# Optimization experiments

Measured on AMD Instinct MI355X. Metric: run time of the kernel, lower is better.

Reference implementation:

```python
import jax, jax.numpy as jnp
import numpy as np

REL_CONTEXT = 0.2  # default forward arg

def setup_inputs() -> dict:
    key = jax.random.key(0)
    ks = jax.random.split(key, 8)
    B, M, D = 4096, 2, 2048
    return {
        "x": jax.random.normal(ks[0], (B, M, D), jnp.float32),
        "sub_type_ids": jax.random.randint(ks[1], (B, M), 0, M),
        "modal_weights": jnp.ones((M,), jnp.float32),
        "emb_table": jax.random.normal(ks[2], (M, D), jnp.float32),
        "Wt": jax.random.normal(ks[3], (D, D), jnp.float32) * (1.0 / np.sqrt(D)),
        "bt": jax.random.normal(ks[4], (D,), jnp.float32) * 0.01,
        "Wrc": jax.random.normal(ks[5], (1, D), jnp.float32) * (1.0 / np.sqrt(D)),
        "brc": jax.random.normal(ks[6], (1,), jnp.float32) * 0.01,
    }

def reference(x, sub_type_ids, modal_weights, emb_table, Wt, bt, Wrc, brc):
    B = x.shape[0]
    D = emb_table.shape[1]
    x = x.reshape(B, -1, D)  # [B, M, D]
    # relational gate: Linear(D->1) on a constant vector filled with 0.2 -> scalar
    rc = jnp.full((D,), REL_CONTEXT, dtype=x.dtype)
    zeta = jax.nn.sigmoid(rc @ Wrc.T + brc)  # [1]
    sub = emb_table[sub_type_ids]  # [B, M, D] embedding lookup
    # fused: per-modality Linear + ReLU (replaces the B*M python loop)
    t = jax.nn.relu(jnp.einsum('bmd,ed->bme', x + sub, Wt) + bt)  # [B, M, D]
    h = modal_weights[None, :, None] * t * zeta[0]
    # dropout is identity in eval mode; final ReLU as in the original
    return jax.nn.relu(h)
```

## Files before the change

kernel.cpp:

```cpp
#include <hip/hip_runtime.h>
#include <hip/hip_bf16.h>
#include <math.h>

#define MROWS 8192
#define KDIM  2048
#define NDIM  2048

#define BM 256
#define BN 128
#define BK 64

typedef short  v8s __attribute__((ext_vector_type(8)));
typedef float  v4f __attribute__((ext_vector_type(4)));

#define A_OFF   0ull
#define W_OFF   ((unsigned long long)MROWS * KDIM * 2ull)
#define MWZ_OFF (W_OFF + (unsigned long long)NDIM * KDIM * 2ull)

__device__ inline unsigned short f2bf(float f) {
    __hip_bfloat16 h = __float2bfloat16(f);
    return *reinterpret_cast<unsigned short*>(&h);
}

__global__ __launch_bounds__(256) void prep_kernel(
    const float* __restrict__ x, const int* __restrict__ ids,
    const float* __restrict__ mw, const float* __restrict__ emb,
    const float* __restrict__ Wrc, const float* __restrict__ brc,
    const float* __restrict__ Wt,
    unsigned short* __restrict__ Abf, unsigned short* __restrict__ Wbf,
    float* __restrict__ mwz)
{
    const int tid = threadIdx.x;

    if (blockIdx.x == 0) {
        __shared__ float red[256];
        float s = 0.f;
        for (int d = tid; d < KDIM; d += 256) s += Wrc[d];
        red[tid] = s;
        __syncthreads();
        for (int off = 128; off > 0; off >>= 1) {
            if (tid < off) red[tid] += red[tid + off];
            __syncthreads();
        }
        if (tid == 0) {
            float zeta = 1.0f / (1.0f + expf(-(0.2f * red[0] + brc[0])));
            mwz[0] = mw[0] * zeta;
            mwz[1] = mw[1] * zeta;
        }
    }

    const int groupsA = MROWS * KDIM / 8;
    for (int g = blockIdx.x * 256 + tid; g < groupsA; g += gridDim.x * 256) {
        const int row = g >> 8;
        const int off = (g & 255) << 3;
        const int st  = ids[row];
        const float4* xp = (const float4*)(x   + (size_t)row * KDIM + off);
        const float4* ep = (const float4*)(emb + (size_t)st  * KDIM + off);
        float4 x0 = xp[0], x1 = xp[1];
        float4 e0 = ep[0], e1 = ep[1];
        v8s o;
        o[0] = (short)f2bf(x0.x + e0.x);
        o[1] = (short)f2bf(x0.y + e0.y);
        o[2] = (short)f2bf(x0.z + e0.z);
        o[3] = (short)f2bf(x0.w + e0.w);
        o[4] = (short)f2bf(x1.x + e1.x);
        o[5] = (short)f2bf(x1.y + e1.y);
        o[6] = (short)f2bf(x1.z + e1.z);
        o[7] = (short)f2bf(x1.w + e1.w);
        *(v8s*)(Abf + (size_t)g * 8) = o;
    }

    const int groupsW = NDIM * KDIM / 8;
    for (int g = blockIdx.x * 256 + tid; g < groupsW; g += gridDim.x * 256) {
        const float4* wp = (const float4*)(Wt + (size_t)g * 8);
        float4 w0 = wp[0], w1 = wp[1];
        v8s o;
        o[0] = (short)f2bf(w0.x); o[1] = (short)f2bf(w0.y);
        o[2] = (short)f2bf(w0.z); o[3] = (short)f2bf(w0.w);
        o[4] = (short)f2bf(w1.x); o[5] = (short)f2bf(w1.y);
        o[6] = (short)f2bf(w1.z); o[7] = (short)f2bf(w1.w);
        *(v8s*)(Wbf + (size_t)g * 8) = o;
    }
}

__global__ __launch_bounds__(256, 2) void gemm_kernel(
    const unsigned short* __restrict__ Abf,
    const unsigned short* __restrict__ Wbf,
    const float* __restrict__ bt,
    const float* __restrict__ mwz,
    float* __restrict__ out)
{
    __shared__ __align__(16) unsigned short lA[BM * BK];
    __shared__ __align__(16) unsigned short lB[BN * BK];

    const int tid  = threadIdx.x;
    const int lane = tid & 63;
    const int wave = tid >> 6;
    const int wr   = wave & 1;
    const int wc   = wave >> 1;
    const int quad = lane >> 4;
    const int mcol = lane & 15;

    const int br = blockIdx.x;
    const int bc = blockIdx.y;

    v4f acc[8][4];
    const v4f vzero = {0.f, 0.f, 0.f, 0.f};
    #pragma unroll
    for (int i = 0; i < 8; i++)
        #pragma unroll
        for (int j = 0; j < 4; j++) acc[i][j] = vzero;

    const unsigned short* gA = Abf + (size_t)(br * BM) * KDIM;
    const unsigned short* gB = Wbf + (size_t)(bc * BN) * KDIM;

    for (int kt = 0; kt < KDIM; kt += BK) {
        #pragma unroll
        for (int q = 0; q < 8; q++) {
            const int f   = q * 256 + tid;
            const int row = f >> 3;
            const int ch  = (f & 7) ^ (row & 7);
            const unsigned short* ga = gA + (size_t)row * KDIM + kt + ch * 8;
            __builtin_amdgcn_global_load_lds(
                (const __attribute__((address_space(1))) void*)ga,
                (__attribute__((address_space(3))) void*)(&lA[(size_t)f * 8]),
                16, 0, 0);
        }
        #pragma unroll
        for (int q = 0; q < 4; q++) {
            const int f   = q * 256 + tid;
            const int row = f >> 3;
            const int ch  = (f & 7) ^ (row & 7);
            const unsigned short* gb = gB + (size_t)row * KDIM + kt + ch * 8;
            __builtin_amdgcn_global_load_lds(
                (const __attribute__((address_space(1))) void*)gb,
                (__attribute__((address_space(3))) void*)(&lB[(size_t)f * 8]),
                16, 0, 0);
        }
        __syncthreads();

        #pragma unroll
        for (int ks = 0; ks < BK; ks += 32) {
            v8s af[8], bf_[4];
            #pragma unroll
            for (int i = 0; i < 8; i++) {
                const int row = wr * 128 + i * 16 + mcol;
                const int cc  = (ks >> 3) + quad;
                const int c   = cc ^ (row & 7);
                af[i] = *(const v8s*)(&lA[row * BK + c * 8]);
            }
            #pragma unroll
            for (int j = 0; j < 4; j++) {
                const int col = wc * 64 + j * 16 + mcol;
                const int cc  = (ks >> 3) + quad;
                const int c   = cc ^ (col & 7);
                bf_[j] = *(const v8s*)(&lB[col * BK + c * 8]);
            }
            #pragma unroll
            for (int i = 0; i < 8; i++)
                #pragma unroll
                for (int j = 0; j < 4; j++)
                    acc[i][j] = __builtin_amdgcn_mfma_f32_16x16x32_bf16(
                        bf_[j], af[i], acc[i][j], 0, 0, 0);
        }
        __syncthreads();
    }

    const float mz = mwz[mcol & 1];
    #pragma unroll
    for (int j = 0; j < 4; j++) {
        const int ncol = bc * BN + wc * 64 + j * 16 + quad * 4;
        const float4 b4 = *(const float4*)(bt + ncol);
        #pragma unroll
        for (int i = 0; i < 8; i++) {
            const int row = br * BM + wr * 128 + i * 16 + mcol;
            float4 o;
            o.x = fmaxf(mz * fmaxf(acc[i][j][0] + b4.x, 0.0f), 0.0f);
            o.y = fmaxf(mz * fmaxf(acc[i][j][1] + b4.y, 0.0f), 0.0f);
            o.z = fmaxf(mz * fmaxf(acc[i][j][2] + b4.z, 0.0f), 0.0f);
            o.w = fmaxf(mz * fmaxf(acc[i][j][3] + b4.w, 0.0f), 0.0f);
            *(float4*)(out + (size_t)row * NDIM + ncol) = o;
        }
    }
}

extern "C" void kernel_launch(void* const* d_in, const int* in_sizes, int n_in,
                              void* d_out, int out_size, void* d_ws, size_t ws_size,
                              hipStream_t stream) {
    const float* x    = (const float*)d_in[0];
    const int*   ids  = (const int*)  d_in[1];
    const float* mw   = (const float*)d_in[2];
    const float* emb  = (const float*)d_in[3];
    const float* Wt   = (const float*)d_in[4];
    const float* bt   = (const float*)d_in[5];
    const float* Wrc  = (const float*)d_in[6];
    const float* brc  = (const float*)d_in[7];
    float* out = (float*)d_out;

    char* ws = (char*)d_ws;
    unsigned short* Abf = (unsigned short*)(ws + A_OFF);
    unsigned short* Wbf = (unsigned short*)(ws + W_OFF);
    float* mwz          = (float*)(ws + MWZ_OFF);

    prep_kernel<<<2048, 256, 0, stream>>>(x, ids, mw, emb, Wrc, brc, Wt,
                                          Abf, Wbf, mwz);

    dim3 grid(MROWS / BM, NDIM / BN);
    gemm_kernel<<<grid, 256, 0, stream>>>(Abf, Wbf, bt, mwz, out);
}
```

Measured before the change: 199.5 us.

## Double-buffer GEMM with 256x256 tiles, phased async loads and block swizzle

Widens the GEMM block tile to 256x256 with 512 threads and double-buffers the LDS tiles. Global-to-LDS loads for tiles t+1 and t+2 are interleaved across four MFMA phases, with explicit vmcnt/lgkmcnt waits and barriers. It also raises wave priority around MFMA bursts and remaps block IDs so neighbouring blocks share rows and columns. The goal is to hide load latency behind compute and cut redundant global traffic. The cost is 128KB of LDS per block, which limits occupancy, and a fragile hand-tuned wait schedule.

New measurement: 231.3 us. +15.9%, slower.

```diff
diff --git a/kernel.cpp b/kernel.cpp
--- a/kernel.cpp
+++ b/kernel.cpp
@@ -7,8 +7,9 @@
 #define NDIM  2048
 
 #define BM 256
-#define BN 128
+#define BN 256
 #define BK 64
+#define NT (KDIM / BK)
 
 typedef short  v8s __attribute__((ext_vector_type(8)));
 typedef float  v4f __attribute__((ext_vector_type(4)));
@@ -83,15 +84,39 @@
     }
 }
 
-__global__ __launch_bounds__(256, 2) void gemm_kernel(
+
+#define SBAR()   __builtin_amdgcn_s_barrier()
+#define LGKM0()  asm volatile("s_waitcnt lgkmcnt(0)" ::: "memory")
+#define VMCNT(n) asm volatile("s_waitcnt vmcnt(" #n ")" ::: "memory")
+
+template<int P>
+__device__ __forceinline__ void mfma_phase(v4f (&acc)[8][4],
+                                           const v8s (&b)[4][2],
+                                           const v8s (&a)[2][2])
+{
+    __builtin_amdgcn_s_setprio(1);
+    #pragma unroll
+    for (int j = 0; j < 4; ++j) {
+        acc[2*P  ][j] = __builtin_amdgcn_mfma_f32_16x16x32_bf16(b[j][0], a[0][0], acc[2*P  ][j], 0, 0, 0);
+        acc[2*P+1][j] = __builtin_amdgcn_mfma_f32_16x16x32_bf16(b[j][0], a[1][0], acc[2*P+1][j], 0, 0, 0);
+    }
+    #pragma unroll
+    for (int j = 0; j < 4; ++j) {
+        acc[2*P  ][j] = __builtin_amdgcn_mfma_f32_16x16x32_bf16(b[j][1], a[0][1], acc[2*P  ][j], 0, 0, 0);
+        acc[2*P+1][j] = __builtin_amdgcn_mfma_f32_16x16x32_bf16(b[j][1], a[1][1], acc[2*P+1][j], 0, 0, 0);
+    }
+    __builtin_amdgcn_s_setprio(0);
+}
+
+__global__ __launch_bounds__(512, 2) void gemm_kernel(
     const unsigned short* __restrict__ Abf,
     const unsigned short* __restrict__ Wbf,
     const float* __restrict__ bt,
     const float* __restrict__ mwz,
     float* __restrict__ out)
 {
-    __shared__ __align__(16) unsigned short lA[BM * BK];
-    __shared__ __align__(16) unsigned short lB[BN * BK];
+    __shared__ __align__(16) unsigned short lA[2][BM * BK];
+    __shared__ __align__(16) unsigned short lB[2][BN * BK];
 
     const int tid  = threadIdx.x;
     const int lane = tid & 63;
@@ -101,8 +126,13 @@
     const int quad = lane >> 4;
     const int mcol = lane & 15;
 
-    const int br = blockIdx.x;
-    const int bc = blockIdx.y;
+    const int flat = (int)blockIdx.x;
+    const int wg   = ((flat & 7) << 5) | (flat >> 3);
+    const int br   = wg & 31;
+    const int bc   = wg >> 5;
+
+    const unsigned short* gA = Abf + (size_t)(br * BM) * KDIM;
+    const unsigned short* gB = Wbf + (size_t)(bc * BN) * KDIM;
 
     v4f acc[8][4];
     const v4f vzero = {0.f, 0.f, 0.f, 0.f};
@@ -111,68 +141,96 @@
         #pragma unroll
         for (int j = 0; j < 4; j++) acc[i][j] = vzero;
 
-    const unsigned short* gA = Abf + (size_t)(br * BM) * KDIM;
-    const unsigned short* gB = Wbf + (size_t)(bc * BN) * KDIM;
-
-    for (int kt = 0; kt < KDIM; kt += BK) {
+    auto stA = [&](int t, int s) {
+        const int f   = (s << 9) + tid;
+        const int row = f >> 3;
+        const int ch  = (f & 7) ^ (row & 7);
+        const unsigned short* g = gA + (size_t)row * KDIM + ((t & 31) << 6) + (ch << 3);
+        __builtin_amdgcn_global_load_lds(
+            (const __attribute__((address_space(1))) void*)g,
+            (__attribute__((address_space(3))) void*)(&lA[t & 1][(size_t)f << 3]),
+            16, 0, 0);
+    };
+    auto stB = [&](int t, int s) {
+        const int f   = (s << 9) + tid;
+        const int row = f >> 3;
+        const int ch  = (f & 7) ^ (row & 7);
+        const unsigned short* g = gB + (size_t)row * KDIM + ((t & 31) << 6) + (ch << 3);
+        __builtin_amdgcn_global_load_lds(
+            (const __attribute__((address_space(1))) void*)g,
+            (__attribute__((address_space(3))) void*)(&lB[t & 1][(size_t)f << 3]),
+            16, 0, 0);
+    };
+
+    auto rdA = [&](const unsigned short* l, int i, int ks) -> v8s {
+        const int row = (wr << 7) + (i << 4) + mcol;
+        const int c   = ((ks << 2) + quad) ^ (row & 7);
+        return *(const v8s*)(l + (row << 6) + (c << 3));
+    };
+    auto rdB = [&](const unsigned short* l, int j, int ks) -> v8s {
+        const int col = (wc << 6) + (j << 4) + mcol;
+        const int c   = ((ks << 2) + quad) ^ (col & 7);
+        return *(const v8s*)(l + (col << 6) + (c << 3));
+    };
+
+    stB(0, 0); stB(0, 1); stB(0, 2); stB(0, 3);
+    stA(0, 0); stA(0, 2);
+    stA(0, 1); stA(0, 3);
+    stB(1, 0); stB(1, 1); stB(1, 2); stB(1, 3);
+    stA(1, 0); stA(1, 2);
+    VMCNT(8);
+    SBAR();
+
+    for (int t = 0; t < NT; ++t) {
+        const unsigned short* cA = &lA[t & 1][0];
+        const unsigned short* cB = &lB[t & 1][0];
+        v8s a[2][2], b[4][2];
+
         #pragma unroll
-        for (int q = 0; q < 8; q++) {
-            const int f   = q * 256 + tid;
-            const int row = f >> 3;
-            const int ch  = (f & 7) ^ (row & 7);
-            const unsigned short* ga = gA + (size_t)row * KDIM + kt + ch * 8;
-            __builtin_amdgcn_global_load_lds(
-                (const __attribute__((address_space(1))) void*)ga,
-                (__attribute__((address_space(3))) void*)(&lA[(size_t)f * 8]),
-                16, 0, 0);
-        }
-        #pragma unroll
-        for (int q = 0; q < 4; q++) {
-            const int f   = q * 256 + tid;
-            const int row = f >> 3;
-            const int ch  = (f & 7) ^ (row & 7);
-            const unsigned short* gb = gB + (size_t)row * KDIM + kt + ch * 8;
-            __builtin_amdgcn_global_load_lds(
-                (const __attribute__((address_space(1))) void*)gb,
-                (__attribute__((address_space(3))) void*)(&lB[(size_t)f * 8]),
-                16, 0, 0);
-        }
-        __syncthreads();
-
-        #pragma unroll
-        for (int ks = 0; ks < BK; ks += 32) {
-            v8s af[8], bf_[4];
-            #pragma unroll
-            for (int i = 0; i < 8; i++) {
-                const int row = wr * 128 + i * 16 + mcol;
-                const int cc  = (ks >> 3) + quad;
-                const int c   = cc ^ (row & 7);
-                af[i] = *(const v8s*)(&lA[row * BK + c * 8]);
-            }
-            #pragma unroll
-            for (int j = 0; j < 4; j++) {
-                const int col = wc * 64 + j * 16 + mcol;
-                const int cc  = (ks >> 3) + quad;
-                const int c   = cc ^ (col & 7);
-                bf_[j] = *(const v8s*)(&lB[col * BK + c * 8]);
-            }
-            #pragma unroll
-            for (int i = 0; i < 8; i++)
-                #pragma unroll
-                for (int j = 0; j < 4; j++)
-                    acc[i][j] = __builtin_amdgcn_mfma_f32_16x16x32_bf16(
-                        bf_[j], af[i], acc[i][j], 0, 0, 0);
-        }
-        __syncthreads();
+        for (int j = 0; j < 4; ++j) {
+            b[j][0] = rdB(cB, j, 0);
+            b[j][1] = rdB(cB, j, 1);
+        }
+        a[0][0] = rdA(cA, 0, 0); a[0][1] = rdA(cA, 0, 1);
+        a[1][0] = rdA(cA, 1, 0); a[1][1] = rdA(cA, 1, 1);
+        stA(t + 1, 1); stA(t + 1, 3);
+        SBAR();
+        mfma_phase<0>(acc, b, a);
+        LGKM0(); SBAR();
+
+        a[0][0] = rdA(cA, 2, 0); a[0][1] = rdA(cA, 2, 1);
+        a[1][0] = rdA(cA, 3, 0); a[1][1] = rdA(cA, 3, 1);
+        stB(t + 2, 0); stB(t + 2, 1);
+        SBAR();
+        mfma_phase<1>(acc, b, a);
+        LGKM0();
+        VMCNT(10);
+        SBAR();
+
+        a[0][0] = rdA(cA, 4, 0); a[0][1] = rdA(cA, 4, 1);
+        a[1][0] = rdA(cA, 5, 0); a[1][1] = rdA(cA, 5, 1);
+        stB(t + 2, 2); stB(t + 2, 3);
+        SBAR();
+        mfma_phase<2>(acc, b, a);
+        LGKM0(); SBAR();
+
+        a[0][0] = rdA(cA, 6, 0); a[0][1] = rdA(cA, 6, 1);
+        a[1][0] = rdA(cA, 7, 0); a[1][1] = rdA(cA, 7, 1);
+        stA(t + 2, 0); stA(t + 2, 2);
+        SBAR();
+        mfma_phase<3>(acc, b, a);
+        LGKM0();
+        VMCNT(8);
+        SBAR();
     }
 
     const float mz = mwz[mcol & 1];
     #pragma unroll
-    for (int j = 0; j < 4; j++) {
+    for (int j = 0; j < 4; ++j) {
         const int ncol = bc * BN + wc * 64 + j * 16 + quad * 4;
         const float4 b4 = *(const float4*)(bt + ncol);
         #pragma unroll
-        for (int i = 0; i < 8; i++) {
+        for (int i = 0; i < 8; ++i) {
             const int row = br * BM + wr * 128 + i * 16 + mcol;
             float4 o;
             o.x = fmaxf(mz * fmaxf(acc[i][j][0] + b4.x, 0.0f), 0.0f);
@@ -205,6 +263,6 @@
     prep_kernel<<<2048, 256, 0, stream>>>(x, ids, mw, emb, Wrc, brc, Wt,
                                           Abf, Wbf, mwz);
 
-    dim3 grid(MROWS / BM, NDIM / BN);
-    gemm_kernel<<<grid, 256, 0, stream>>>(Abf, Wbf, bt, mwz, out);
-}
+    dim3 grid(MROWS / BM * (NDIM / BN));
+    gemm_kernel<<<grid, 512, 0, stream>>>(Abf, Wbf, bt, mwz, out);
+}
```

## Double-buffer LDS tiles with prefetch and shrink GEMM tile to 128x128x32

Applied to the files above, without the earlier changes.

Moves the bf16 GEMM to a two-stage LDS double buffer. The next K-tile is issued via global_load_lds before computing the current one, and only one barrier is used per K step. The block tile drops from 256x128x64 to 128x128x32 with launch bounds raised to 4 blocks per CU, a new XOR swizzle, precomputed LDS offsets, and s_setprio around the MFMA burst. The aim is to overlap global loads with MFMA work and raise occupancy. The cost is less reuse per tile, more K iterations, and twice as many blocks.

Measured after the change: 223.0 us. 1.12x slower.

```diff
diff --git a/kernel.cpp b/kernel.cpp
--- a/kernel.cpp
+++ b/kernel.cpp
@@ -6,9 +6,10 @@
 #define KDIM  2048
 #define NDIM  2048
 
-#define BM 256
+#define BM 128
 #define BN 128
-#define BK 64
+#define BK 32
+#define NT (KDIM / BK)
 
 typedef short  v8s __attribute__((ext_vector_type(8)));
 typedef float  v4f __attribute__((ext_vector_type(4)));
@@ -83,97 +84,132 @@
     }
 }
 
-__global__ __launch_bounds__(256, 2) void gemm_kernel(
+
+#define SBAR()   __builtin_amdgcn_s_barrier()
+#define LGKM0()  asm volatile("s_waitcnt lgkmcnt(0)" ::: "memory")
+#define VMCNT0() asm volatile("s_waitcnt vmcnt(0)" ::: "memory")
+
+#define GLDS(gp, lp)                                                      \
+    __builtin_amdgcn_global_load_lds(                                     \
+        (const __attribute__((address_space(1))) void*)(gp),              \
+        (__attribute__((address_space(3))) void*)(lp), 16, 0, 0)
+
+__global__ __launch_bounds__(256, 4) void gemm_kernel(
     const unsigned short* __restrict__ Abf,
     const unsigned short* __restrict__ Wbf,
     const float* __restrict__ bt,
     const float* __restrict__ mwz,
     float* __restrict__ out)
 {
-    __shared__ __align__(16) unsigned short lA[BM * BK];
-    __shared__ __align__(16) unsigned short lB[BN * BK];
+    __shared__ __align__(16) unsigned short lA0[BM * BK];
+    __shared__ __align__(16) unsigned short lA1[BM * BK];
+    __shared__ __align__(16) unsigned short lB0[BN * BK];
+    __shared__ __align__(16) unsigned short lB1[BN * BK];
 
     const int tid  = threadIdx.x;
     const int lane = tid & 63;
     const int wave = tid >> 6;
-    const int wr   = wave & 1;
-    const int wc   = wave >> 1;
+    const int wm   = wave & 1;
+    const int wn   = wave >> 1;
     const int quad = lane >> 4;
     const int mcol = lane & 15;
 
     const int br = blockIdx.x;
     const int bc = blockIdx.y;
 
-    v4f acc[8][4];
+    const unsigned short* gA = Abf + (size_t)(br * BM) * KDIM;
+    const unsigned short* gB = Wbf + (size_t)(bc * BN) * KDIM;
+
+    const int f0 = tid,        r0 = f0 >> 2, c0 = (f0 & 3) ^ ((r0 >> 1) & 3);
+    const int f1 = 256 + tid,  r1 = f1 >> 2, c1 = (f1 & 3) ^ ((r1 >> 1) & 3);
+    const int gOff0 = r0 * KDIM + c0 * 8;
+    const int gOff1 = r1 * KDIM + c1 * 8;
+    const int lOff0 = f0 * 8;
+    const int lOff1 = f1 * 8;
+
+    int aOff[4], bOff[4];
+    #pragma unroll
+    for (int i = 0; i < 4; ++i) {
+        const int r = wm * 64 + i * 16 + mcol;
+        aOff[i] = r * BK + (quad ^ ((r >> 1) & 3)) * 8;
+    }
+    #pragma unroll
+    for (int j = 0; j < 4; ++j) {
+        const int c = wn * 64 + j * 16 + mcol;
+        bOff[j] = c * BK + (quad ^ ((c >> 1) & 3)) * 8;
+    }
+
+    v4f acc[4][4];
     const v4f vzero = {0.f, 0.f, 0.f, 0.f};
     #pragma unroll
-    for (int i = 0; i < 8; i++)
+    for (int i = 0; i < 4; i++)
         #pragma unroll
         for (int j = 0; j < 4; j++) acc[i][j] = vzero;
 
-    const unsigned short* gA = Abf + (size_t)(br * BM) * KDIM;
-    const unsigned short* gB = Wbf + (size_t)(bc * BN) * KDIM;
-
-    for (int kt = 0; kt < KDIM; kt += BK) {
-        #pragma unroll
-        for (int q = 0; q < 8; q++) {
-            const int f   = q * 256 + tid;
-            const int row = f >> 3;
-            const int ch  = (f & 7) ^ (row & 7);
-            const unsigned short* ga = gA + (size_t)row * KDIM + kt + ch * 8;
-            __builtin_amdgcn_global_load_lds(
-                (const __attribute__((address_space(1))) void*)ga,
-                (__attribute__((address_space(3))) void*)(&lA[(size_t)f * 8]),
-                16, 0, 0);
-        }
-        #pragma unroll
-        for (int q = 0; q < 4; q++) {
-            const int f   = q * 256 + tid;
-            const int row = f >> 3;
-            const int ch  = (f & 7) ^ (row & 7);
-            const unsigned short* gb = gB + (size_t)row * KDIM + kt + ch * 8;
-            __builtin_amdgcn_global_load_lds(
-                (const __attribute__((address_space(1))) void*)gb,
-                (__attribute__((address_space(3))) void*)(&lB[(size_t)f * 8]),
-                16, 0, 0);
-        }
-        __syncthreads();
-
-        #pragma unroll
-        for (int ks = 0; ks < BK; ks += 32) {
-            v8s af[8], bf_[4];
-            #pragma unroll
-            for (int i = 0; i < 8; i++) {
-                const int row = wr * 128 + i * 16 + mcol;
-                const int cc  = (ks >> 3) + quad;
-                const int c   = cc ^ (row & 7);
-                af[i] = *(const v8s*)(&lA[row * BK + c * 8]);
-            }
-            #pragma unroll
-            for (int j = 0; j < 4; j++) {
-                const int col = wc * 64 + j * 16 + mcol;
-                const int cc  = (ks >> 3) + quad;
-                const int c   = cc ^ (col & 7);
-                bf_[j] = *(const v8s*)(&lB[col * BK + c * 8]);
-            }
-            #pragma unroll
-            for (int i = 0; i < 8; i++)
-                #pragma unroll
-                for (int j = 0; j < 4; j++)
-                    acc[i][j] = __builtin_amdgcn_mfma_f32_16x16x32_bf16(
-                        bf_[j], af[i], acc[i][j], 0, 0, 0);
-        }
-        __syncthreads();
+#define STAGE(NA, NB, T)                                                  \
+    do {                                                                  \
+        const int kt = (T) << 5;                                          \
+        GLDS(gA + gOff0 + kt, NA + lOff0);                                \
+        GLDS(gA + gOff1 + kt, NA + lOff1);                                \
+        GLDS(gB + gOff0 + kt, NB + lOff0);                                \
+        GLDS(gB + gOff1 + kt, NB + lOff1);                                \
+    } while (0)
+
+#define COMPUTE(CA, CB)                                                   \
+    do {                                                                  \
+        v8s a0 = *(const v8s*)((CA) + aOff[0]);                           \
+        v8s a1 = *(const v8s*)((CA) + aOff[1]);                           \
+        v8s a2 = *(const v8s*)((CA) + aOff[2]);                           \
+        v8s a3 = *(const v8s*)((CA) + aOff[3]);                           \
+        v8s b0 = *(const v8s*)((CB) + bOff[0]);                           \
+        v8s b1 = *(const v8s*)((CB) + bOff[1]);                           \
+        v8s b2 = *(const v8s*)((CB) + bOff[2]);                           \
+        v8s b3 = *(const v8s*)((CB) + bOff[3]);                           \
+        __builtin_amdgcn_s_setprio(1);                                    \
+        acc[0][0] = __builtin_amdgcn_mfma_f32_16x16x32_bf16(b0, a0, acc[0][0], 0, 0, 0); \
+        acc[1][0] = __builtin_amdgcn_mfma_f32_16x16x32_bf16(b0, a1, acc[1][0], 0, 0, 0); \
+        acc[2][0] = __builtin_amdgcn_mfma_f32_16x16x32_bf16(b0, a2, acc[2][0], 0, 0, 0); \
+        acc[3][0] = __builtin_amdgcn_mfma_f32_16x16x32_bf16(b0, a3, acc[3][0], 0, 0, 0); \
+        acc[0][1] = __builtin_amdgcn_mfma_f32_16x16x32_bf16(b1, a0, acc[0][1], 0, 0, 0); \
+        acc[1][1] = __builtin_amdgcn_mfma_f32_16x16x32_bf16(b1, a1, acc[1][1], 0, 0, 0); \
+        acc[2][1] = __builtin_amdgcn_mfma_f32_16x16x32_bf16(b1, a2, acc[2][1], 0, 0, 0); \
+        acc[3][1] = __builtin_amdgcn_mfma_f32_16x16x32_bf16(b1, a3, acc[3][1], 0, 0, 0); \
+        acc[0][2] = __builtin_amdgcn_mfma_f32_16x16x32_bf16(b2, a0, acc[0][2], 0, 0, 0); \
+        acc[1][2] = __builtin_amdgcn_mfma_f32_16x16x32_bf16(b2, a1, acc[1][2], 0, 0, 0); \
+        acc[2][2] = __builtin_amdgcn_mfma_f32_16x16x32_bf16(b2, a2, acc[2][2], 0, 0, 0); \
+        acc[3][2] = __builtin_amdgcn_mfma_f32_16x16x32_bf16(b2, a3, acc[3][2], 0, 0, 0); \
+        acc[0][3] = __builtin_amdgcn_mfma_f32_16x16x32_bf16(b3, a0, acc[0][3], 0, 0, 0); \
+        acc[1][3] = __builtin_amdgcn_mfma_f32_16x16x32_bf16(b3, a1, acc[1][3], 0, 0, 0); \
+        acc[2][3] = __builtin_amdgcn_mfma_f32_16x16x32_bf16(b3, a2, acc[2][3], 0, 0, 0); \
+        acc[3][3] = __builtin_amdgcn_mfma_f32_16x16x32_bf16(b3, a3, acc[3][3], 0, 0, 0); \
+        __builtin_amdgcn_s_setprio(0);                                    \
+    } while (0)
+
+#define KT(CA, CB, NA, NB, T)                                             \
+    {                                                                     \
+        if ((T) + 1 < NT) STAGE(NA, NB, (T) + 1);                         \
+        COMPUTE(CA, CB);                                                  \
+        LGKM0(); VMCNT0(); SBAR();                                        \
+    }
+
+    STAGE(lA0, lB0, 0);
+    VMCNT0();
+    SBAR();
+
+    #pragma unroll 1
+    for (int tt = 0; tt < NT; tt += 2) {
+        KT(lA0, lB0, lA1, lB1, tt);
+        KT(lA1, lB1, lA0, lB0, tt + 1);
     }
 
     const float mz = mwz[mcol & 1];
     #pragma unroll
-    for (int j = 0; j < 4; j++) {
-        const int ncol = bc * BN + wc * 64 + j * 16 + quad * 4;
+    for (int j = 0; j < 4; ++j) {
+        const int ncol = bc * BN + wn * 64 + j * 16 + quad * 4;
         const float4 b4 = *(const float4*)(bt + ncol);
         #pragma unroll
-        for (int i = 0; i < 8; i++) {
-            const int row = br * BM + wr * 128 + i * 16 + mcol;
+        for (int i = 0; i < 4; ++i) {
+            const int row = br * BM + wm * 64 + i * 16 + mcol;
             float4 o;
             o.x = fmaxf(mz * fmaxf(acc[i][j][0] + b4.x, 0.0f), 0.0f);
             o.y = fmaxf(mz * fmaxf(acc[i][j][1] + b4.y, 0.0f), 0.0f);
@@ -182,6 +218,10 @@
             *(float4*)(out + (size_t)row * NDIM + ncol) = o;
         }
     }
+
+#undef KT
+#undef COMPUTE
+#undef STAGE
 }
 
 extern "C" void kernel_launch(void* const* d_in, const int* in_sizes, int n_in,
```
